# Optimization experiments

Measured on AMD Instinct MI355X. Metric: run time of the kernel, lower is better.

The kernel has to match this reference:

```python
import jax, jax.numpy as jnp
import numpy as np

N, D, K = 16384, 256, 4096  # encoded vectors, embedding_dim, codebook_size


def setup_inputs() -> dict:
    key = jax.random.key(0)
    k_ze, k_cb = jax.random.split(key)
    ze = jax.random.normal(k_ze, (N, D), dtype=jnp.float32)
    codebook = jax.random.normal(k_cb, (K, D), dtype=jnp.float32)
    return {"ze": ze, "codebook": codebook}


def reference(ze, codebook):
    # Pairwise squared distances: ||ze||^2 + ||e||^2 - 2 ze e^T  -> [N, K]
    sq_norm = (
        jnp.sum(ze ** 2, axis=-1, keepdims=True)
        + jnp.sum(codebook ** 2, axis=1)
        - 2.0 * jnp.matmul(ze, codebook.T)
    )
    indices = jnp.argmin(sq_norm, axis=-1)            # [N]
    zq = jnp.take(codebook, indices, axis=0)          # [N, D] gather

    # VQ losses (stop-gradient mirrors .detach())
    vq_e_loss = jnp.mean((zq - jax.lax.stop_gradient(ze)) ** 2)
    vq_commit_loss = jnp.mean((jax.lax.stop_gradient(zq) - ze) ** 2)

    # perplexity: probs[i] = count_i / 10 (faithful to original, incl. /10)
    counts = jnp.zeros((K,), dtype=jnp.float32).at[indices].add(1.0)
    probs = counts / 10.0
    perplexity = jnp.exp(-jnp.sum(probs * jnp.log(probs + 1e-10)))

    return indices, zq, vq_e_loss, vq_commit_loss, perplexity
```

## Files before the change

### kernel.cpp

```cpp
#include <hip/hip_runtime.h>
#include <math.h>

#define N_TOT 16384
#define DIM   256
#define KCB   4096

typedef __attribute__((ext_vector_type(8)))  short s8v;
typedef __attribute__((ext_vector_type(16))) float f16v;

#define LOSS_OFF  32768
#define DONE_OFF  32772
#define GDONE_OFF 33284
#define PK_OFF    33344
#define CBF_OFF   164416
#define WS_NEED   4358720ull
#define ZERO_W    37008

__device__ __forceinline__ void gload16(const void* g, void* l) {
  __builtin_amdgcn_global_load_lds(
      (const __attribute__((address_space(1))) unsigned int*)g,
      (__attribute__((address_space(3))) unsigned int*)l, 16, 0, 0);
}

__global__ __launch_bounds__(256)
void cb_prep_k(const float* __restrict__ cb, float* __restrict__ ws) {
  __shared__ float Cf[32 * 260];
  const int t = threadIdx.x, tile = blockIdx.x;
  for (int i = tile * 256 + t; i < ZERO_W; i += 128 * 256) ws[KCB + i] = 0.0f;

  const int c0 = tile * 32;
  {
    int r = t >> 3, q = t & 7;
    const float4* src4 = (const float4*)(cb + (size_t)(c0 + r) * DIM);
    float4* dst = (float4*)&Cf[r * 260];
    #pragma unroll
    for (int i = 0; i < 8; ++i) dst[q + 8 * i] = src4[q + 8 * i];
  }
  __syncthreads();

  const int col = t >> 3, j = t & 7;
  ushort* tb = (ushort*)((char*)ws + CBF_OFF) + (size_t)tile * 16384;
  const float* rowp = Cf + col * 260;
  float s = 0.0f;
  #pragma unroll
  for (int ks = 0; ks < 16; ++ks) {
    #pragma unroll
    for (int kh = 0; kh < 2; ++kh) {
      float x = rowp[ks * 16 + kh * 8 + j];
      s += x * x;
      unsigned xb = __float_as_uint(x);
      unsigned hb = xb & 0xFFFF0000u;
      float lf = x - __uint_as_float(hb);
      tb[ks * 512 + kh * 256 + t]        = (ushort)(xb >> 16);
      tb[8192 + ks * 512 + kh * 256 + t] = (ushort)(__float_as_uint(lf) >> 16);
    }
  }
  s += __shfl_down(s, 4, 8);
  s += __shfl_down(s, 2, 8);
  s += __shfl_down(s, 1, 8);
  if (j == 0) ws[c0 + col] = s;
}

__global__ __launch_bounds__(256, 2)
void vq_mfma_k(const float* __restrict__ ze, const float* __restrict__ cb,
               float* __restrict__ ws, float* __restrict__ out) {
  __shared__ __align__(16) char ldsU[66560];
  __shared__ int flagLast;

  const int t    = threadIdx.x;
  const int lane = t & 63;
  const int w    = t >> 6;
  const int ln31 = lane & 31;
  const int hl   = lane >> 5;
  const int cq   = blockIdx.x >> 7;
  const int mb   = blockIdx.x & 127;
  const int m0   = mb * 128;

  const float* cbn = ws;
  unsigned long long* pk = (unsigned long long*)((char*)ws + PK_OFF);
  const char* cbF = (const char*)ws + CBF_OFF;

  s8v ah[16], al[16];
  float* Af = (float*)ldsU;
  #pragma unroll 1
  for (int ph = 0; ph < 2; ++ph) {
    __syncthreads();
    {
      int r = t >> 2, q = t & 3;
      const float4* src4 = (const float4*)(ze + (size_t)(m0 + ph * 64 + r) * DIM);
      float4* dst = (float4*)&Af[r * 260];
      #pragma unroll
      for (int i = 0; i < 16; ++i) dst[q + 4 * i] = src4[q + 4 * i];
    }
    __syncthreads();
    if ((w >> 1) == ph) {
      int rl = (w & 1) * 32 + ln31;
      const float* rowp = Af + rl * 260;
      #pragma unroll
      for (int ks = 0; ks < 16; ++ks) {
        float4 x0 = *(const float4*)(rowp + ks * 16 + hl * 8);
        float4 x1 = *(const float4*)(rowp + ks * 16 + hl * 8 + 4);
        float xs[8] = {x0.x, x0.y, x0.z, x0.w, x1.x, x1.y, x1.z, x1.w};
        #pragma unroll
        for (int j = 0; j < 8; ++j) {
          unsigned xb = __float_as_uint(xs[j]);
          unsigned hb = xb & 0xFFFF0000u;
          float lf = xs[j] - __uint_as_float(hb);
          ah[ks][j] = (short)(xb >> 16);
          al[ks][j] = (short)(__float_as_uint(lf) >> 16);
        }
      }
    }
  }
  __syncthreads();

  char* bufs0 = ldsU;
  char* bufs1 = ldsU + 32768;
  const char* qbase = cbF + (size_t)cq * 32 * 32768;

  {
    const char* g = qbase + (size_t)w * 1024 + (size_t)lane * 16;
    #pragma unroll
    for (int ii = 0; ii < 8; ++ii) gload16(g + ii * 4096, bufs0 + w * 1024 + ii * 4096);
  }

  float cvn = cbn[cq * 1024 + ln31];

  float best[16];
  int   bidx[16];
  #pragma unroll
  for (int r = 0; r < 16; ++r) { best[r] = -1e30f; bidx[r] = 0; }

  #pragma unroll 1
  for (int tt = 0; tt < 32; ++tt) {
    __syncthreads();
    if (tt + 1 < 32) {
      const char* g = qbase + (size_t)(tt + 1) * 32768 + (size_t)w * 1024 + (size_t)lane * 16;
      char* lp = ((tt + 1) & 1 ? bufs1 : bufs0) + w * 1024;
      #pragma unroll
      for (int ii = 0; ii < 8; ++ii) gload16(g + ii * 4096, lp + ii * 4096);
    }

    const float half_cv = 0.5f * cvn;
    if (tt + 1 < 32) cvn = cbn[cq * 1024 + (tt + 1) * 32 + ln31];
    const char* bc = (tt & 1) ? bufs1 : bufs0;

    f16v hh, xx;
    #pragma unroll
    for (int r = 0; r < 16; ++r) { hh[r] = 0.0f; xx[r] = 0.0f; }

    #pragma unroll
    for (int ks = 0; ks < 16; ++ks) {
      s8v bh = *(const s8v*)(bc + ks * 1024 + lane * 16);
      s8v bl = *(const s8v*)(bc + 16384 + ks * 1024 + lane * 16);
      hh = __builtin_amdgcn_mfma_f32_32x32x16_bf16(ah[ks], bh, hh, 0, 0, 0);
      xx = __builtin_amdgcn_mfma_f32_32x32x16_bf16(ah[ks], bl, xx, 0, 0, 0);
      xx = __builtin_amdgcn_mfma_f32_32x32x16_bf16(al[ks], bh, xx, 0, 0, 0);
    }

    const int c0 = cq * 1024 + tt * 32 + ln31;
    #pragma unroll
    for (int r = 0; r < 16; ++r) {
      float s = hh[r] + xx[r] - half_cv;
      if (s > best[r]) { best[r] = s; bidx[r] = c0; }
    }
  }

  #pragma unroll
  for (int r = 0; r < 16; ++r) {
    float s = best[r];
    int   c = bidx[r];
    #pragma unroll
    for (int mk = 1; mk < 32; mk <<= 1) {
      float os = __shfl_xor(s, mk, 64);
      int   oc = __shfl_xor(c, mk, 64);
      if (os > s || (os == s && oc < c)) { s = os; c = oc; }
    }
    if (ln31 == 0) {
      int row = m0 + w * 32 + (r & 3) + 8 * (r >> 2) + 4 * hl;
      unsigned u = __float_as_uint(s);
      unsigned enc = (u & 0x80000000u) ? ~u : (u | 0x80000000u);
      unsigned long long p = ((unsigned long long)enc << 32) | (unsigned)(KCB - 1 - c);
      atomicMax(&pk[row], p);
    }
  }

  __threadfence();
  unsigned* done  = (unsigned*)((char*)ws + DONE_OFF);
  unsigned* gdone = (unsigned*)((char*)ws + GDONE_OFF);
  if (t == 0) flagLast = (atomicAdd(&done[mb], 1u) == 3u) ? 1 : 0;
  __syncthreads();
  if (!flagLast) return;
  __threadfence();

  int*   sIdx     = (int*)ldsU;
  float* counts   = ws + KCB;
  float* loss_sum = ws + LOSS_OFF / 4;

  if (t < 128) {
    unsigned long long p = atomicMax(&pk[m0 + t], 0ull);
    int col = KCB - 1 - (int)(unsigned)(p & 0xFFFFFFFFull);
    out[m0 + t] = (float)col;
    sIdx[t] = col;
    atomicAdd(&counts[col], 1.0f);
  }
  __syncthreads();

  float* out_zq = out + N_TOT;
  float lsum = 0.0f;
  #pragma unroll 4
  for (int p = 0; p < 32; ++p) {
    int r = w + 4 * p;
    float4 cvv = *(const float4*)(cb + (size_t)sIdx[r] * DIM + lane * 4);
    float4 zv  = *(const float4*)(ze + (size_t)(m0 + r) * DIM + lane * 4);
    *(float4*)(out_zq + (size_t)(m0 + r) * DIM + lane * 4) = cvv;
    float dx = cvv.x - zv.x, dy = cvv.y - zv.y, dz = cvv.z - zv.z, dw = cvv.w - zv.w;
    lsum += dx * dx + dy * dy + dz * dz + dw * dw;
  }
  #pragma unroll
  for (int off = 32; off > 0; off >>= 1) lsum += __shfl_down(lsum, off, 64);
  if (lane == 0) atomicAdd(loss_sum, lsum);

  __threadfence();
  if (t == 0) flagLast = (atomicAdd(gdone, 1u) == 127u) ? 1 : 0;
  __syncthreads();
  if (!flagLast) return;
  __threadfence();

  float* red = (float*)(ldsU + 2048);
  float s = 0.0f;
  #pragma unroll
  for (int k = t; k < KCB; k += 256) {
    float c = atomicAdd(&counts[k], 0.0f);
    float pr = c * 0.1f;
    s += pr * logf(pr + 1e-10f);
  }
  red[t] = s;
  __syncthreads();
  for (int q = 128; q > 0; q >>= 1) { if (t < q) red[t] += red[t + q]; __syncthreads(); }
  if (t == 0) {
    float loss = atomicAdd(loss_sum, 0.0f) / (float)((size_t)N_TOT * DIM);
    float* o = out + N_TOT + (size_t)N_TOT * DIM;
    o[0] = loss;
    o[1] = loss;
    o[2] = expf(-red[0]);
  }
}

__global__ void zero_ws_k(float* __restrict__ ws, int nw) {
  int i = blockIdx.x * 256 + threadIdx.x;
  if (i < nw) ws[KCB + i] = 0.0f;
}

__global__ void cbnorm_k(const float* __restrict__ cb, float* __restrict__ ws) {
  int row  = blockIdx.x * 4 + (threadIdx.x >> 6);
  int lane = threadIdx.x & 63;
  float4 v = *(const float4*)(cb + (size_t)row * DIM + lane * 4);
  float s = v.x*v.x + v.y*v.y + v.z*v.z + v.w*v.w;
  #pragma unroll
  for (int off = 32; off > 0; off >>= 1) s += __shfl_down(s, off, 64);
  if (lane == 0) ws[row] = s;
}

#define FBM 32
#define FBN 64
#define FBD 128
__global__ __launch_bounds__(256, 4)
void vq_main_k(const float* __restrict__ ze, const float* __restrict__ cb,
               float* __restrict__ ws, float* __restrict__ out) {
  __shared__ float As[FBM * FBD];
  __shared__ float Bs[FBN * FBD];
  __shared__ float red_d[FBM * 16];
  __shared__ int   red_i[FBM * 16];
  __shared__ int   sIdx[FBM];

  const int t  = threadIdx.x;
  const int tx = t & 15;
  const int ty = t >> 4;
  const int m0 = blockIdx.x * FBM;

  const float* cbn = ws;
  float* counts    = ws + KCB;
  float* loss_sum  = ws + 2 * KCB;

  float best0 = 1e30f, best1 = 1e30f;
  int   bidx0 = 0,     bidx1 = 0;
  const int sA = ty & 7;
  const int sB = tx & 7;

  for (int kt = 0; kt < KCB / FBN; ++kt) {
    float cbnj[4];
    #pragma unroll
    for (int j = 0; j < 4; ++j) cbnj[j] = cbn[kt * FBN + tx + 16 * j];
    float acc[2][4];
    #pragma unroll
    for (int i = 0; i < 2; ++i)
      #pragma unroll
      for (int j = 0; j < 4; ++j) acc[i][j] = 0.0f;

    for (int dc = 0; dc < DIM / FBD; ++dc) {
      __syncthreads();
      {
        int c  = t & 31;
        int rb = t >> 5;
        #pragma unroll
        for (int p = 0; p < 4; ++p) {
          int r = rb + 8 * p;
          float4 v = *(const float4*)(ze + (size_t)(m0 + r) * DIM + dc * FBD + c * 4);
          *(float4*)&As[r * FBD + ((c ^ (r & 7)) << 2)] = v;
        }
        #pragma unroll
        for (int p = 0; p < 8; ++p) {
          int r = rb + 8 * p;
          float4 v = *(const float4*)(cb + (size_t)(kt * FBN + r) * DIM + dc * FBD + c * 4);
          *(float4*)&Bs[r * FBD + ((c ^ (r & 7)) << 2)] = v;
        }
      }
      __syncthreads();
      #pragma unroll 8
      for (int ds = 0; ds < FBD / 4; ++ds) {
        float4 a0 = *(const float4*)&As[ty * FBD + ((ds ^ sA) << 2)];
        float4 a1 = *(const float4*)&As[(ty + 16) * FBD + ((ds ^ sA) << 2)];
        float4 b[4];
        #pragma unroll
        for (int j = 0; j < 4; ++j)
          b[j] = *(const float4*)&Bs[(tx + 16 * j) * FBD + ((ds ^ sB) << 2)];
        #pragma unroll
        for (int j = 0; j < 4; ++j) {
          acc[0][j] = fmaf(a0.x, b[j].x, acc[0][j]);
          acc[0][j] = fmaf(a0.y, b[j].y, acc[0][j]);
          acc[0][j] = fmaf(a0.z, b[j].z, acc[0][j]);
          acc[0][j] = fmaf(a0.w, b[j].w, acc[0][j]);
          acc[1][j] = fmaf(a1.x, b[j].x, acc[1][j]);
          acc[1][j] = fmaf(a1.y, b[j].y, acc[1][j]);
          acc[1][j] = fmaf(a1.z, b[j].z, acc[1][j]);
          acc[1][j] = fmaf(a1.w, b[j].w, acc[1][j]);
        }
      }
    }
    #pragma unroll
    for (int j = 0; j < 4; ++j) {
      int kg = kt * FBN + tx + 16 * j;
      float d0 = cbnj[j] - 2.0f * acc[0][j];
      float d1 = cbnj[j] - 2.0f * acc[1][j];
      if (d0 < best0) { best0 = d0; bidx0 = kg; }
      if (d1 < best1) { best1 = d1; bidx1 = kg; }
    }
  }

  __syncthreads();
  red_d[ty * 16 + tx] = best0;        red_i[ty * 16 + tx] = bidx0;
  red_d[(ty + 16) * 16 + tx] = best1; red_i[(ty + 16) * 16 + tx] = bidx1;
  __syncthreads();

  if (t < FBM) {
    float bd = red_d[t * 16]; int bi = red_i[t * 16];
    #pragma unroll
    for (int q = 1; q < 16; ++q) {
      float d = red_d[t * 16 + q]; int i2 = red_i[t * 16 + q];
      if (d < bd || (d == bd && i2 < bi)) { bd = d; bi = i2; }
    }
    out[m0 + t] = (float)bi;
    sIdx[t] = bi;
    atomicAdd(&counts[bi], 1.0f);
  }
  __syncthreads();

  float* out_zq = out + N_TOT;
  const int wv = t >> 6, ln = t & 63;
  float lsum = 0.0f;
  #pragma unroll
  for (int p = 0; p < 8; ++p) {
    int r = wv + 4 * p;
    float4 cvv = *(const float4*)(cb + (size_t)sIdx[r] * DIM + ln * 4);
    float4 zv  = *(const float4*)(ze + (size_t)(m0 + r) * DIM + ln * 4);
    *(float4*)(out_zq + (size_t)(m0 + r) * DIM + ln * 4) = cvv;
    float dx = cvv.x - zv.x, dy = cvv.y - zv.y, dz = cvv.z - zv.z, dw = cvv.w - zv.w;
    lsum += dx*dx + dy*dy + dz*dz + dw*dw;
  }
  #pragma unroll
  for (int off = 32; off > 0; off >>= 1) lsum += __shfl_down(lsum, off, 64);
  if (ln == 0) atomicAdd(loss_sum, lsum);
}

__global__ void finalize_k(const float* __restrict__ ws, float* __restrict__ out) {
  __shared__ float red[256];
  int t = threadIdx.x;
  const float* counts = ws + KCB;
  float s = 0.0f;
  for (int k = t; k < KCB; k += 256) {
    float p = counts[k] * 0.1f;
    s += p * logf(p + 1e-10f);
  }
  red[t] = s;
  __syncthreads();
  for (int q = 128; q > 0; q >>= 1) { if (t < q) red[t] += red[t + q]; __syncthreads(); }
  if (t == 0) {
    float loss = ws[2 * KCB] / (float)((size_t)N_TOT * DIM);
    float* o = out + N_TOT + (size_t)N_TOT * DIM;
    o[0] = loss;
    o[1] = loss;
    o[2] = expf(-red[0]);
  }
}

extern "C" void kernel_launch(void* const* d_in, const int* in_sizes, int n_in,
                              void* d_out, int out_size, void* d_ws, size_t ws_size,
                              hipStream_t stream) {
  const float* ze = (const float*)d_in[0];
  const float* cb = (const float*)d_in[1];
  float* out = (float*)d_out;
  float* ws  = (float*)d_ws;

  if (ws_size >= WS_NEED) {
    cb_prep_k<<<128, 256, 0, stream>>>(cb, ws);
    vq_mfma_k<<<512, 256, 0, stream>>>(ze, cb, ws, out);
  } else {
    zero_ws_k<<<(KCB + 1 + 255) / 256, 256, 0, stream>>>(ws, KCB + 1);
    cbnorm_k<<<KCB / 4, 256, 0, stream>>>(cb, ws);
    vq_main_k<<<N_TOT / FBM, 256, 0, stream>>>(ze, cb, ws, out);
    finalize_k<<<1, 256, 0, stream>>>(ws, out);
  }
}
```

Baseline: 225.4 us.

## Split gather/loss epilogue into separate kernel and vectorize codebook prep

Removes the per-row-block completion counter from the MFMA kernel. The gather, loss and perplexity tail now runs in a new 512-block kernel that reads the packed argmin results after a kernel boundary instead of relying on last-block atomics. The codebook prep kernel is rewritten to use 256 blocks with direct float4 loads and packed 16-byte bf16 hi/lo stores, with no LDS staging. This adds a kernel launch in exchange for better parallelism in the tail and cheaper synchronization.

```diff
diff --git a/kernel.cpp b/kernel.cpp
--- a/kernel.cpp
+++ b/kernel.cpp
@@ -9,7 +9,6 @@
 typedef __attribute__((ext_vector_type(16))) float f16v;
 
 #define LOSS_OFF  32768
-#define DONE_OFF  32772
 #define GDONE_OFF 33284
 #define PK_OFF    33344
 #define CBF_OFF   164416
@@ -24,48 +23,58 @@
 
 __global__ __launch_bounds__(256)
 void cb_prep_k(const float* __restrict__ cb, float* __restrict__ ws) {
-  __shared__ float Cf[32 * 260];
-  const int t = threadIdx.x, tile = blockIdx.x;
-  for (int i = tile * 256 + t; i < ZERO_W; i += 128 * 256) ws[KCB + i] = 0.0f;
-
-  const int c0 = tile * 32;
+  __shared__ float sn[256];
+  const int t = threadIdx.x;
+  const int tile = blockIdx.x >> 1;
+  const int ch   = blockIdx.x & 1;
   {
-    int r = t >> 3, q = t & 7;
-    const float4* src4 = (const float4*)(cb + (size_t)(c0 + r) * DIM);
-    float4* dst = (float4*)&Cf[r * 260];
-    #pragma unroll
-    for (int i = 0; i < 8; ++i) dst[q + 8 * i] = src4[q + 8 * i];
-  }
-  __syncthreads();
-
-  const int col = t >> 3, j = t & 7;
+    int i = blockIdx.x * 256 + t;
+    if (i < ZERO_W) ws[KCB + i] = 0.0f;
+  }
+
+  const int col = t & 15;
+  const int kk  = t >> 4;
+  const int gc  = ch * 16 + col;
+  const int row = tile * 32 + gc;
   ushort* tb = (ushort*)((char*)ws + CBF_OFF) + (size_t)tile * 16384;
-  const float* rowp = Cf + col * 260;
+  const float* src = cb + (size_t)row * DIM;
+
   float s = 0.0f;
   #pragma unroll
-  for (int ks = 0; ks < 16; ++ks) {
-    #pragma unroll
-    for (int kh = 0; kh < 2; ++kh) {
-      float x = rowp[ks * 16 + kh * 8 + j];
-      s += x * x;
-      unsigned xb = __float_as_uint(x);
+  for (int it = 0; it < 2; ++it) {
+    const int pp = kk + 16 * it;
+    const int ks = pp >> 1, kh = pp & 1;
+    float4 x0 = *(const float4*)(src + ks * 16 + kh * 8);
+    float4 x1 = *(const float4*)(src + ks * 16 + kh * 8 + 4);
+    float xs[8] = {x0.x, x0.y, x0.z, x0.w, x1.x, x1.y, x1.z, x1.w};
+    unsigned h[8], l[8];
+    #pragma unroll
+    for (int j = 0; j < 8; ++j) {
+      s += xs[j] * xs[j];
+      unsigned xb = __float_as_uint(xs[j]);
       unsigned hb = xb & 0xFFFF0000u;
-      float lf = x - __uint_as_float(hb);
-      tb[ks * 512 + kh * 256 + t]        = (ushort)(xb >> 16);
-      tb[8192 + ks * 512 + kh * 256 + t] = (ushort)(__float_as_uint(lf) >> 16);
-    }
-  }
-  s += __shfl_down(s, 4, 8);
-  s += __shfl_down(s, 2, 8);
-  s += __shfl_down(s, 1, 8);
-  if (j == 0) ws[c0 + col] = s;
+      float lf = xs[j] - __uint_as_float(hb);
+      h[j] = xb >> 16;
+      l[j] = __float_as_uint(lf) >> 16;
+    }
+    *(uint4*)&tb[ks * 512 + kh * 256 + gc * 8] =
+        make_uint4(h[0] | (h[1] << 16), h[2] | (h[3] << 16), h[4] | (h[5] << 16), h[6] | (h[7] << 16));
+    *(uint4*)&tb[8192 + ks * 512 + kh * 256 + gc * 8] =
+        make_uint4(l[0] | (l[1] << 16), l[2] | (l[3] << 16), l[4] | (l[5] << 16), l[6] | (l[7] << 16));
+  }
+  sn[col * 16 + kk] = s;
+  __syncthreads();
+  if (t < 16) {
+    float acc = 0.0f;
+    #pragma unroll
+    for (int q = 0; q < 16; ++q) acc += sn[t * 16 + q];
+    ws[tile * 32 + ch * 16 + t] = acc;
+  }
 }
 
 __global__ __launch_bounds__(256, 2)
-void vq_mfma_k(const float* __restrict__ ze, const float* __restrict__ cb,
-               float* __restrict__ ws, float* __restrict__ out) {
+void vq_mfma_k(const float* __restrict__ ze, float* __restrict__ ws) {
   __shared__ __align__(16) char ldsU[66560];
-  __shared__ int flagLast;
 
   const int t    = threadIdx.x;
   const int lane = t & 63;
@@ -184,21 +193,23 @@
       atomicMax(&pk[row], p);
     }
   }
-
-  __threadfence();
-  unsigned* done  = (unsigned*)((char*)ws + DONE_OFF);
-  unsigned* gdone = (unsigned*)((char*)ws + GDONE_OFF);
-  if (t == 0) flagLast = (atomicAdd(&done[mb], 1u) == 3u) ? 1 : 0;
-  __syncthreads();
-  if (!flagLast) return;
-  __threadfence();
-
-  int*   sIdx     = (int*)ldsU;
+}
+
+__global__ __launch_bounds__(256)
+void gather_fin_k(const float* __restrict__ ze, const float* __restrict__ cb,
+                  float* __restrict__ ws, float* __restrict__ out) {
+  __shared__ int   sIdx[32];
+  __shared__ float red[256];
+  __shared__ int   flagLast;
+  const int t  = threadIdx.x;
+  const int m0 = blockIdx.x * 32;
   float* counts   = ws + KCB;
   float* loss_sum = ws + LOSS_OFF / 4;
-
-  if (t < 128) {
-    unsigned long long p = atomicMax(&pk[m0 + t], 0ull);
+  unsigned* gdone = (unsigned*)((char*)ws + GDONE_OFF);
+  const unsigned long long* pk = (const unsigned long long*)((const char*)ws + PK_OFF);
+
+  if (t < 32) {
+    unsigned long long p = pk[m0 + t];
     int col = KCB - 1 - (int)(unsigned)(p & 0xFFFFFFFFull);
     out[m0 + t] = (float)col;
     sIdx[t] = col;
@@ -207,27 +218,28 @@
   __syncthreads();
 
   float* out_zq = out + N_TOT;
+  const int w = t >> 6, ln = t & 63;
   float lsum = 0.0f;
-  #pragma unroll 4
-  for (int p = 0; p < 32; ++p) {
+  #pragma unroll
+  for (int p = 0; p < 8; ++p) {
     int r = w + 4 * p;
-    float4 cvv = *(const float4*)(cb + (size_t)sIdx[r] * DIM + lane * 4);
-    float4 zv  = *(const float4*)(ze + (size_t)(m0 + r) * DIM + lane * 4);
-    *(float4*)(out_zq + (size_t)(m0 + r) * DIM + lane * 4) = cvv;
+    float4 cvv = *(const float4*)(cb + (size_t)sIdx[r] * DIM + ln * 4);
+    float4 zv  = *(const float4*)(ze + (size_t)(m0 + r) * DIM + ln * 4);
+    *(float4*)(out_zq + (size_t)(m0 + r) * DIM + ln * 4) = cvv;
     float dx = cvv.x - zv.x, dy = cvv.y - zv.y, dz = cvv.z - zv.z, dw = cvv.w - zv.w;
     lsum += dx * dx + dy * dy + dz * dz + dw * dw;
   }
   #pragma unroll
   for (int off = 32; off > 0; off >>= 1) lsum += __shfl_down(lsum, off, 64);
-  if (lane == 0) atomicAdd(loss_sum, lsum);
-
+  if (ln == 0) atomicAdd(loss_sum, lsum);
+
+  __syncthreads();
   __threadfence();
-  if (t == 0) flagLast = (atomicAdd(gdone, 1u) == 127u) ? 1 : 0;
+  if (t == 0) flagLast = (atomicAdd(gdone, 1u) == 511u) ? 1 : 0;
   __syncthreads();
   if (!flagLast) return;
   __threadfence();
 
-  float* red = (float*)(ldsU + 2048);
   float s = 0.0f;
   #pragma unroll
   for (int k = t; k < KCB; k += 256) {
@@ -413,8 +425,9 @@
   float* ws  = (float*)d_ws;
 
   if (ws_size >= WS_NEED) {
-    cb_prep_k<<<128, 256, 0, stream>>>(cb, ws);
-    vq_mfma_k<<<512, 256, 0, stream>>>(ze, cb, ws, out);
+    cb_prep_k<<<256, 256, 0, stream>>>(cb, ws);
+    vq_mfma_k<<<512, 256, 0, stream>>>(ze, ws);
+    gather_fin_k<<<512, 256, 0, stream>>>(ze, cb, ws, out);
   } else {
     zero_ws_k<<<(KCB + 1 + 255) / 256, 256, 0, stream>>>(ws, KCB + 1);
     cbnorm_k<<<KCB / 4, 256, 0, stream>>>(cb, ws);
```

Result: slower. 246.9 us (+9.5%).
